# Kernel tuning notes

Measured on AMD Instinct MI355X. Metric: run time of the kernel, lower is better.

The kernel has to match this reference:

```python
import jax, jax.numpy as jnp
import numpy as np

N_NODES = 100000
NEG_SLOPE = 0.2


def glorot(key, shape):
    fan_in, fan_out = shape[0], shape[-1]
    lim = jnp.sqrt(6.0 / (fan_in + fan_out))
    return jax.random.uniform(key, shape, jnp.float32, -lim, lim)


def setup_inputs() -> dict:
    key = jax.random.key(0)
    ks = jax.random.split(key, 16)
    x = jax.random.normal(ks[0], (N_NODES, 128), jnp.float32)
    edge_index = jax.random.randint(ks[1], (2, 1600000), 0, N_NODES, jnp.int64)
    H1, C1 = 4, 32
    C2 = 64
    return {
        "x": x,
        "edge_index": edge_index,
        # layer 1: GATv2Conv(128 -> 32, heads=4, concat)
        "Wl1": glorot(ks[2], (128, H1 * C1)), "bl1": jnp.zeros((H1 * C1,), jnp.float32),
        "Wr1": glorot(ks[3], (128, H1 * C1)), "br1": jnp.zeros((H1 * C1,), jnp.float32),
        "att1": glorot(ks[4], (H1, C1)),
        "bias1": jnp.zeros((H1 * C1,), jnp.float32),
        # layer 2: GATv2Conv(128 -> 64, heads=1, concat)
        "Wl2": glorot(ks[5], (H1 * C1, C2)), "bl2": jnp.zeros((C2,), jnp.float32),
        "Wr2": glorot(ks[6], (H1 * C1, C2)), "br2": jnp.zeros((C2,), jnp.float32),
        "att2": glorot(ks[7], (1, C2)),
        "bias2": jnp.zeros((C2,), jnp.float32),
    }


def gatv2_layer(x, src, dst, Wl, bl, Wr, br, att, bias):
    # x: [N, F_in]; src/dst: [E] (self-loops already appended)
    H, C = att.shape
    n = x.shape[0]
    xl = (x @ Wl + bl).reshape(n, H, C)  # source transform
    xr = (x @ Wr + br).reshape(n, H, C)  # target transform
    e = jax.nn.leaky_relu(xl[src] + xr[dst], NEG_SLOPE)          # [E, H, C]
    score = jnp.einsum('ehc,hc->eh', e, att)                     # [E, H]
    # segment softmax over incoming edges of each destination node
    smax = jax.ops.segment_max(score, dst, num_segments=n)       # [N, H]
    ex = jnp.exp(score - smax[dst])
    denom = jax.ops.segment_sum(ex, dst, num_segments=n)
    alpha = ex / denom[dst]                                      # [E, H]
    out = jax.ops.segment_sum(alpha[:, :, None] * xl[src], dst, num_segments=n)
    return out.reshape(n, H * C) + bias


def reference(x, edge_index, Wl1, bl1, Wr1, br1, att1, bias1,
              Wl2, bl2, Wr2, br2, att2, bias2):
    n = x.shape[0]
    loops = jnp.arange(n, dtype=edge_index.dtype)
    src = jnp.concatenate([edge_index[0], loops])
    dst = jnp.concatenate([edge_index[1], loops])
    h = gatv2_layer(x, src, dst, Wl1, bl1, Wr1, br1, att1, bias1)
    h = jax.nn.relu(h)
    out = gatv2_layer(h, src, dst, Wl2, bl2, Wr2, br2, att2, bias2)
    return out
```

## Files before the change

### kernel.cpp

```cpp
#include <hip/hip_runtime.h>
#include <hip/hip_fp16.h>

#define NEG 0.2f

typedef _Float16 f16x8 __attribute__((ext_vector_type(8)));
typedef _Float16 f16x2 __attribute__((ext_vector_type(2)));
typedef float    f32x4 __attribute__((ext_vector_type(4)));

__device__ __forceinline__ float fdot2h(__half2 a, __half2 b, float c) {
    return __builtin_amdgcn_fdot2(__builtin_bit_cast(f16x2, a),
                                  __builtin_bit_cast(f16x2, b), c, false);
}

__device__ __forceinline__ __half2 u2h2(unsigned int u) {
    return __builtin_bit_cast(__half2, u);
}

__device__ __forceinline__ __half2 hmax2(__half2 a, __half2 b) {
    unsigned int ua = __builtin_bit_cast(unsigned int, a);
    unsigned int ub = __builtin_bit_cast(unsigned int, b);
    unsigned int ud;
    asm("v_pk_max_f16 %0, %1, %2" : "=v"(ud) : "v"(ua), "v"(ub));
    return __builtin_bit_cast(__half2, ud);
}

template<int CTRL>
__device__ __forceinline__ float dppadd(float x) {
    int xi = __builtin_bit_cast(int, x);
    int yi = __builtin_amdgcn_update_dpp(0, xi, CTRL, 0xf, 0xf, true);
    return x + __builtin_bit_cast(float, yi);
}

template<int CGRP, int CPW, bool IN_F16, bool HPL>
__global__ __launch_bounds__(256) void xform_k(
    const float* __restrict__ Xf, const __half* __restrict__ Xh,
    const float* __restrict__ Wl, const float* __restrict__ bl,
    const float* __restrict__ Wr, const float* __restrict__ br,
    __half* __restrict__ YL, __half* __restrict__ YR, int nrows)
{
    __shared__ _Float16 Ws[CGRP * 136];

    const int t  = threadIdx.x;
    const int c0 = blockIdx.y * CGRP;

    for (int i = t; i < 128 * CGRP; i += 256) {
        int k = i / CGRP, cl = i % CGRP;
        int gc = c0 + cl;
        const float* Wp = (gc >= CPW) ? Wr : Wl;
        int lc = gc - ((gc >= CPW) ? CPW : 0);
        Ws[cl * 136 + k] = (_Float16)Wp[(long)k * CPW + lc];
    }
    __syncthreads();

    const int lane = t & 63, wv = t >> 6;
    const int m = lane & 15, quad = lane >> 4;

    const int ntiles = (nrows + 15) >> 4;
    const int stride = gridDim.x * 4;

    int tile = blockIdx.x * 4 + wv;
    if (tile >= ntiles) return;

    f16x8 A0[4], A1[4];

    auto loadA = [&](int tl, f16x8* Af) {
        int row = tl * 16 + m;
        if (row >= nrows) row = nrows - 1;
        if constexpr (IN_F16) {
            const uint4* Xp = (const uint4*)(Xh + (long)row * 128);
            #pragma unroll
            for (int ks = 0; ks < 4; ++ks) {
                uint4 v = Xp[ks * 4 + quad];
                Af[ks] = __builtin_bit_cast(f16x8, v);
            }
        } else {
            const float4* Xp = (const float4*)(Xf + (long)row * 128);
            #pragma unroll
            for (int ks = 0; ks < 4; ++ks) {
                float4 a = Xp[ks * 8 + quad * 2];
                float4 b = Xp[ks * 8 + quad * 2 + 1];
                _Float16 h[8] = {(_Float16)a.x,(_Float16)a.y,(_Float16)a.z,(_Float16)a.w,
                                 (_Float16)b.x,(_Float16)b.y,(_Float16)b.z,(_Float16)b.w};
                Af[ks] = *(f16x8*)h;
            }
        }
    };

    loadA(tile, A0);

    for (; tile < ntiles; tile += stride) {
        int nt = tile + stride;
        if (nt < ntiles) loadA(nt, A1);

        const int r = tile * 16 + m;
        const bool rv = r < nrows;

        #pragma unroll
        for (int ct = 0; ct < CGRP / 16; ++ct) {
            f32x4 acc = (f32x4){0.f, 0.f, 0.f, 0.f};
            #pragma unroll
            for (int ks = 0; ks < 4; ++ks) {
                f16x8 Bf = *(const f16x8*)&Ws[(ct * 16 + m) * 136 + ks * 32 + quad * 8];
                acc = __builtin_amdgcn_mfma_f32_16x16x32_f16(Bf, A0[ks], acc, 0, 0, 0);
            }
            int colb = c0 + ct * 16 + quad * 4;
            int which = colb >= CPW;
            int lcb = colb - (which ? CPW : 0);
            const float* bp = (which ? br : bl) + lcb;
            float4 bb = *(const float4*)bp;
            if (rv) {
                _Float16 h4[4] = { (_Float16)(acc[0] + bb.x), (_Float16)(acc[1] + bb.y),
                                   (_Float16)(acc[2] + bb.z), (_Float16)(acc[3] + bb.w) };
                _Float16* Y = (_Float16*)(which ? YR : YL);
                long idx;
                if (HPL && !which)
                    idx = (long)(lcb >> 6) * ((long)nrows * 64) + (long)r * 64 + (lcb & 63);
                else
                    idx = (long)r * CPW + lcb;
                *(uint2*)&Y[idx] = *(uint2*)h4;
            }
        }
        #pragma unroll
        for (int ks = 0; ks < 4; ++ks) A0[ks] = A1[ks];
    }
}

__global__ __launch_bounds__(256) void h1_k(
    const int* __restrict__ ei, int* __restrict__ gh, int E0, int ET, int NBK)
{
    __shared__ int h[256];
    const int t = threadIdx.x, blk = blockIdx.x;
    h[t] = 0;
    __syncthreads();
    int e = blk * 4096 + t;
    #pragma unroll
    for (int u = 0; u < 16; ++u, e += 256) {
        if (e < ET) {
            int dst = (e < E0) ? ei[E0 + e] : (e - E0);
            atomicAdd(&h[dst >> 9], 1);
        }
    }
    __syncthreads();
    gh[t * NBK + blk] = h[t];
}

__global__ __launch_bounds__(256) void scan1_k(
    const int* __restrict__ cnt, int* __restrict__ loc, int* __restrict__ bsum, int n)
{
    __shared__ int wsum[4];
    int t = threadIdx.x;
    int i0 = blockIdx.x * 1024 + t * 4;
    int4 v;
    v.x = (i0 + 0 < n) ? cnt[i0 + 0] : 0;
    v.y = (i0 + 1 < n) ? cnt[i0 + 1] : 0;
    v.z = (i0 + 2 < n) ? cnt[i0 + 2] : 0;
    v.w = (i0 + 3 < n) ? cnt[i0 + 3] : 0;
    int tsum = v.x + v.y + v.z + v.w;
    int incl = tsum;
    #pragma unroll
    for (int s = 1; s < 64; s <<= 1) {
        int u = __shfl_up(incl, s, 64);
        if ((t & 63) >= s) incl += u;
    }
    int wid = t >> 6;
    if ((t & 63) == 63) wsum[wid] = incl;
    __syncthreads();
    int woff = 0;
    #pragma unroll
    for (int w = 0; w < 4; ++w) if (w < wid) woff += wsum[w];
    int ex = woff + incl - tsum;
    if (i0 + 0 < n) loc[i0 + 0] = ex;
    if (i0 + 1 < n) loc[i0 + 1] = ex + v.x;
    if (i0 + 2 < n) loc[i0 + 2] = ex + v.x + v.y;
    if (i0 + 3 < n) loc[i0 + 3] = ex + v.x + v.y + v.z;
    if (t == 255) bsum[blockIdx.x] = woff + incl;
}

__global__ void scan2_k(const int* __restrict__ bsum, int* __restrict__ bcarry,
                        int M, int* __restrict__ total_out)
{
    int lane = threadIdx.x;
    int carry = 0;
    for (int base = 0; base < M; base += 64) {
        int i = base + lane;
        int v = (i < M) ? bsum[i] : 0;
        int incl = v;
        #pragma unroll
        for (int s = 1; s < 64; s <<= 1) {
            int u = __shfl_up(incl, s, 64);
            if (lane >= s) incl += u;
        }
        if (i < M) bcarry[i] = carry + incl - v;
        carry += __shfl(incl, 63, 64);
    }
    if (lane == 0) *total_out = carry;
}

__global__ __launch_bounds__(256) void scan3_k(
    int* __restrict__ off, const int* __restrict__ bcarry, int n)
{
    int i = blockIdx.x * 256 + threadIdx.x;
    if (i >= n) return;
    off[i] += bcarry[i >> 10];
}

__global__ __launch_bounds__(256) void sc1_k(
    const int* __restrict__ ei, const int* __restrict__ gh,
    uint2* __restrict__ rec, int E0, int ET, int NBK)
{
    __shared__ int lofs[256];
    const int t = threadIdx.x, blk = blockIdx.x;
    lofs[t] = gh[t * NBK + blk];
    __syncthreads();
    int e = blk * 4096 + t;
    #pragma unroll
    for (int u = 0; u < 16; ++u, e += 256) {
        if (e < ET) {
            int src = (e < E0) ? ei[e]      : (e - E0);
            int dst = (e < E0) ? ei[E0 + e] : (e - E0);
            int p = atomicAdd(&lofs[dst >> 9], 1);
            rec[p] = make_uint2((unsigned)src, (unsigned)dst);
        }
    }
}

__global__ __launch_bounds__(256) void p2_k(
    const uint2* __restrict__ rec, const int* __restrict__ gh,
    int* __restrict__ srcs, int* __restrict__ off, int N, int NBK)
{
    __shared__ int hist[512];
    __shared__ int sc[2][512];
    __shared__ int curo[512];
    const int t = threadIdx.x;
    const int b = blockIdx.x;
    const int base = gh[b * NBK];
    const int end  = gh[(b + 1) * NBK];
    hist[t] = 0; hist[t + 256] = 0;
    __syncthreads();
    for (int i = base + t; i < end; i += 256) {
        uint2 r = rec[i];
        atomicAdd(&hist[r.y & 511], 1);
    }
    __syncthreads();
    sc[0][t] = hist[t]; sc[0][t + 256] = hist[t + 256];
    __syncthreads();
    int pp = 0;
    for (int s = 1; s < 512; s <<= 1, pp ^= 1) {
        int j0 = t, j1 = t + 256;
        sc[pp ^ 1][j0] = sc[pp][j0] + ((j0 >= s) ? sc[pp][j0 - s] : 0);
        sc[pp ^ 1][j1] = sc[pp][j1] + ((j1 >= s) ? sc[pp][j1 - s] : 0);
        __syncthreads();
    }
    {
        int j0 = t, j1 = t + 256;
        int e0 = base + sc[pp][j0] - hist[j0];
        int e1 = base + sc[pp][j1] - hist[j1];
        curo[j0] = e0;
        curo[j1] = e1;
        int d0 = b * 512 + j0, d1 = b * 512 + j1;
        if (d0 < N) off[d0] = e0;
        if (d1 < N) off[d1] = e1;
    }
    __syncthreads();
    for (int i = base + t; i < end; i += 256) {
        uint2 r = rec[i];
        int pos = atomicAdd(&curo[r.y & 511], 1);
        srcs[pos] = (int)r.x;
    }
}

template<bool RELU>
__global__ __launch_bounds__(256) void fused128hp_k(
    const __half* __restrict__ XLp, const __half* __restrict__ XR,
    const float* __restrict__ ATT, const int* __restrict__ srcs,
    const int* __restrict__ off, const float* __restrict__ bias,
    __half* __restrict__ OUT, int N, int p)
{
    const int t   = threadIdx.x;
    const int d   = blockIdx.x * 32 + (t >> 3);
    const int sub = t & 7;
    const bool nv = d < N;

    int a = 0, b = 0;
    if (nv) { a = off[d]; b = off[d + 1]; }

    __half2 xr[4] = { u2h2(0), u2h2(0), u2h2(0), u2h2(0) };
    if (nv) {
        uint4 ur = *(const uint4*)(XR + (long)d * 128 + p * 64 + sub * 8);
        xr[0] = u2h2(ur.x); xr[1] = u2h2(ur.y); xr[2] = u2h2(ur.z); xr[3] = u2h2(ur.w);
    }
    float4 at0f = ((const float4*)ATT)[p * 16 + sub * 2];
    float4 at1f = ((const float4*)ATT)[p * 16 + sub * 2 + 1];
    __half2 at[4] = { __floats2half2_rn(at0f.x, at0f.y), __floats2half2_rn(at0f.z, at0f.w),
                      __floats2half2_rn(at1f.x, at1f.y), __floats2half2_rn(at1f.z, at1f.w) };
    const __half2 neg2 = __float2half2_rn(NEG);

    float l = 0.f;
    float accv[8] = {0.f,0.f,0.f,0.f,0.f,0.f,0.f,0.f};

    const uint4* XL4 = (const uint4*)(XLp + (size_t)p * N * 64);

    if (b > a) {
        const int bm1 = b - 1;
        int sA = srcs[a];
        uint4 r0 = XL4[(long)sA * 8 + sub];
        int i1 = (a + 1 < bm1) ? a + 1 : bm1;
        int sB = srcs[i1];
        uint4 r1 = XL4[(long)sB * 8 + sub];
        int i2 = (a + 2 < bm1) ? a + 2 : bm1;
        int s2 = srcs[i2];

        for (int e = a; e < b; ++e) {
            uint4 r2 = XL4[(long)s2 * 8 + sub];
            int i3 = (e + 3 < bm1) ? e + 3 : bm1;
            int s3 = srcs[i3];

            __half2 x0 = u2h2(r0.x), x1 = u2h2(r0.y), x2 = u2h2(r0.z), x3 = u2h2(r0.w);
            __half2 s0h = __hadd2(x0, xr[0]);
            __half2 s1h = __hadd2(x1, xr[1]);
            __half2 s2h = __hadd2(x2, xr[2]);
            __half2 s3h = __hadd2(x3, xr[3]);
            __half2 q0 = hmax2(s0h, __hmul2(s0h, neg2));
            __half2 q1 = hmax2(s1h, __hmul2(s1h, neg2));
            __half2 q2 = hmax2(s2h, __hmul2(s2h, neg2));
            __half2 q3 = hmax2(s3h, __hmul2(s3h, neg2));
            float p0 = fdot2h(q0, at[0], 0.f);
            p0 = fdot2h(q1, at[1], p0);
            p0 = fdot2h(q2, at[2], p0);
            p0 = fdot2h(q3, at[3], p0);
            p0 = dppadd<0xB1>(p0);
            p0 = dppadd<0x4E>(p0);
            float ex = __expf(p0);
            l += ex;
            float2 f0 = __half22float2(x0), f1 = __half22float2(x1);
            float2 f2 = __half22float2(x2), f3 = __half22float2(x3);
            accv[0] += ex * f0.x; accv[1] += ex * f0.y;
            accv[2] += ex * f1.x; accv[3] += ex * f1.y;
            accv[4] += ex * f2.x; accv[5] += ex * f2.y;
            accv[6] += ex * f3.x; accv[7] += ex * f3.y;

            r0 = r1; r1 = r2; s2 = s3;
        }
    }

    if (nv) {
        float inv = 1.f / l;
        float4 b0 = ((const float4*)bias)[p * 16 + sub * 2];
        float4 b1 = ((const float4*)bias)[p * 16 + sub * 2 + 1];
        float o[8] = { accv[0]*inv + b0.x, accv[1]*inv + b0.y,
                       accv[2]*inv + b0.z, accv[3]*inv + b0.w,
                       accv[4]*inv + b1.x, accv[5]*inv + b1.y,
                       accv[6]*inv + b1.z, accv[7]*inv + b1.w };
        if constexpr (RELU) {
            #pragma unroll
            for (int j = 0; j < 8; ++j) o[j] = fmaxf(o[j], 0.f);
        }
        uint4 uo;
        uo.x = __builtin_bit_cast(unsigned int, __floats2half2_rn(o[0], o[1]));
        uo.y = __builtin_bit_cast(unsigned int, __floats2half2_rn(o[2], o[3]));
        uo.z = __builtin_bit_cast(unsigned int, __floats2half2_rn(o[4], o[5]));
        uo.w = __builtin_bit_cast(unsigned int, __floats2half2_rn(o[6], o[7]));
        *(uint4*)(OUT + (long)d * 128 + p * 64 + sub * 8) = uo;
    }
}

template<bool RELU>
__global__ __launch_bounds__(256) void fused64_k(
    const __half* __restrict__ XL, const __half* __restrict__ XR,
    const float* __restrict__ ATT, const int* __restrict__ srcs,
    const int* __restrict__ off, const float* __restrict__ bias,
    float* __restrict__ OUT, int N)
{
    const int t   = threadIdx.x;
    const int d   = blockIdx.x * 32 + (t >> 3);
    const int sub = t & 7;
    const bool nv = d < N;

    int a = 0, b = 0;
    if (nv) { a = off[d]; b = off[d + 1]; }

    __half2 xr[4] = { u2h2(0), u2h2(0), u2h2(0), u2h2(0) };
    if (nv) {
        uint4 ur = *(const uint4*)(XR + (long)d * 64 + sub * 8);
        xr[0] = u2h2(ur.x); xr[1] = u2h2(ur.y); xr[2] = u2h2(ur.z); xr[3] = u2h2(ur.w);
    }
    float4 at0f = ((const float4*)ATT)[sub * 2];
    float4 at1f = ((const float4*)ATT)[sub * 2 + 1];
    __half2 at[4] = { __floats2half2_rn(at0f.x, at0f.y), __floats2half2_rn(at0f.z, at0f.w),
                      __floats2half2_rn(at1f.x, at1f.y), __floats2half2_rn(at1f.z, at1f.w) };
    const __half2 neg2 = __float2half2_rn(NEG);

    float l = 0.f;
    float accv[8] = {0.f,0.f,0.f,0.f,0.f,0.f,0.f,0.f};

    const uint4* XL4 = (const uint4*)XL;

    if (b > a) {
        const int bm1 = b - 1;
        int sA = srcs[a];
        uint4 r0 = XL4[(long)sA * 8 + sub];
        int i1 = (a + 1 < bm1) ? a + 1 : bm1;
        int sB = srcs[i1];
        uint4 r1 = XL4[(long)sB * 8 + sub];
        int i2 = (a + 2 < bm1) ? a + 2 : bm1;
        int s2 = srcs[i2];

        for (int e = a; e < b; ++e) {
            uint4 r2 = XL4[(long)s2 * 8 + sub];
            int i3 = (e + 3 < bm1) ? e + 3 : bm1;
            int s3 = srcs[i3];

            __half2 x0 = u2h2(r0.x), x1 = u2h2(r0.y), x2 = u2h2(r0.z), x3 = u2h2(r0.w);
            __half2 s0h = __hadd2(x0, xr[0]);
            __half2 s1h = __hadd2(x1, xr[1]);
            __half2 s2h = __hadd2(x2, xr[2]);
            __half2 s3h = __hadd2(x3, xr[3]);
            __half2 q0 = hmax2(s0h, __hmul2(s0h, neg2));
            __half2 q1 = hmax2(s1h, __hmul2(s1h, neg2));
            __half2 q2 = hmax2(s2h, __hmul2(s2h, neg2));
            __half2 q3 = hmax2(s3h, __hmul2(s3h, neg2));
            float p0 = fdot2h(q0, at[0], 0.f);
            p0 = fdot2h(q1, at[1], p0);
            p0 = fdot2h(q2, at[2], p0);
            p0 = fdot2h(q3, at[3], p0);
            p0 = dppadd<0xB1>(p0);
            p0 = dppadd<0x4E>(p0);
            p0 = dppadd<0x141>(p0);
            float ex = __expf(p0);
            l += ex;
            float2 f0 = __half22float2(x0), f1 = __half22float2(x1);
            float2 f2 = __half22float2(x2), f3 = __half22float2(x3);
            accv[0] += ex * f0.x; accv[1] += ex * f0.y;
            accv[2] += ex * f1.x; accv[3] += ex * f1.y;
            accv[4] += ex * f2.x; accv[5] += ex * f2.y;
            accv[6] += ex * f3.x; accv[7] += ex * f3.y;

            r0 = r1; r1 = r2; s2 = s3;
        }
    }

    if (nv) {
        float inv = 1.f / l;
        float4 b0 = ((const float4*)bias)[sub * 2];
        float4 b1 = ((const float4*)bias)[sub * 2 + 1];
        float4 o0 = make_float4(accv[0]*inv + b0.x, accv[1]*inv + b0.y,
                                accv[2]*inv + b0.z, accv[3]*inv + b0.w);
        float4 o1 = make_float4(accv[4]*inv + b1.x, accv[5]*inv + b1.y,
                                accv[6]*inv + b1.z, accv[7]*inv + b1.w);
        if constexpr (RELU) {
            o0.x = fmaxf(o0.x, 0.f); o0.y = fmaxf(o0.y, 0.f);
            o0.z = fmaxf(o0.z, 0.f); o0.w = fmaxf(o0.w, 0.f);
            o1.x = fmaxf(o1.x, 0.f); o1.y = fmaxf(o1.y, 0.f);
            o1.z = fmaxf(o1.z, 0.f); o1.w = fmaxf(o1.w, 0.f);
        }
        *(float4*)(OUT + (long)d * 64 + sub * 8)     = o0;
        *(float4*)(OUT + (long)d * 64 + sub * 8 + 4) = o1;
    }
}

extern "C" void kernel_launch(void* const* d_in, const int* in_sizes, int n_in,
                              void* d_out, int out_size, void* d_ws, size_t ws_size,
                              hipStream_t stream)
{
    const float* x     = (const float*)d_in[0];
    const int*   ei    = (const int*)  d_in[1];
    const float* Wl1   = (const float*)d_in[2];
    const float* bl1   = (const float*)d_in[3];
    const float* Wr1   = (const float*)d_in[4];
    const float* br1   = (const float*)d_in[5];
    const float* att1  = (const float*)d_in[6];
    const float* bias1 = (const float*)d_in[7];
    const float* Wl2   = (const float*)d_in[8];
    const float* bl2   = (const float*)d_in[9];
    const float* Wr2   = (const float*)d_in[10];
    const float* br2   = (const float*)d_in[11];
    const float* att2  = (const float*)d_in[12];
    const float* bias2 = (const float*)d_in[13];

    const int  N  = in_sizes[0] / 128;
    const int  E0 = in_sizes[1] / 2;
    const int  ET = E0 + N;

    char* w = (char*)d_ws;
    __half* XLh = (__half*)w;
    __half* XRh = XLh + (size_t)N * 128;
    __half* Cch = XRh + (size_t)N * 128;
    int*    off = (int*)(Cch + (size_t)N * 128);
    int*    srcs= off + (N + 1);
    int*    gh  = srcs + ET;
    uint2*  rec = (uint2*)w;
    float*  out = (float*)d_out;

    dim3 b256(256);
    const int ng32  = (N + 31) / 32;

    const int NBK   = (ET + 4095) / 4096;
    const int n1    = 256 * NBK;
    const int NB1   = (n1 + 1023) / 1024;
    const int NBUCK = (N + 511) / 512;
    int* bsum = gh + n1;
    int* bcar = bsum + NB1;

    h1_k<<<NBK, b256, 0, stream>>>(ei, gh, E0, ET, NBK);
    scan1_k<<<NB1, b256, 0, stream>>>(gh, gh, bsum, n1);
    scan2_k<<<1, 64, 0, stream>>>(bsum, bcar, NB1, off + N);
    scan3_k<<<(n1 + 255) / 256, b256, 0, stream>>>(gh, bcar, n1);
    sc1_k<<<NBK, b256, 0, stream>>>(ei, gh, rec, E0, ET, NBK);
    p2_k<<<NBUCK, b256, 0, stream>>>(rec, gh, srcs, off, N, NBK);

    xform_k<128, 128, false, true><<<dim3(512, 2), b256, 0, stream>>>(
        x, nullptr, Wl1, bl1, Wr1, br1, XLh, XRh, N);
    fused128hp_k<true><<<ng32, b256, 0, stream>>>(XLh, XRh, att1, srcs, off, bias1, Cch, N, 0);
    fused128hp_k<true><<<ng32, b256, 0, stream>>>(XLh, XRh, att1, srcs, off, bias1, Cch, N, 1);

    xform_k<128, 64, true, false><<<dim3(1024, 1), b256, 0, stream>>>(
        nullptr, Cch, Wl2, bl2, Wr2, br2, XLh, XRh, N);
    fused64_k<false><<<ng32, b256, 0, stream>>>(XLh, XRh, att2, srcs, off, bias2, out, N);
}
```

Measured before the change: 380.1 us.

## Compute all output columns per block in xform and deepen A prefetch

The layer-1 transform now computes all 256 output columns (Wl and Wr) in one block instead of splitting the columns across two grid rows. Each X tile is therefore read once instead of twice. The weight staging uses float4 loads and a 140-element LDS row pitch, and the A-fragment prefetch goes from one tile ahead to two. The cost is more LDS per block (about 70KB for layer 1) and more registers, which can lower occupancy. The layer-2 grid is also halved to 512 blocks.

```diff
diff --git a/kernel.cpp b/kernel.cpp
--- a/kernel.cpp
+++ b/kernel.cpp
@@ -31,24 +31,27 @@
     return x + __builtin_bit_cast(float, yi);
 }
 
-template<int CGRP, int CPW, bool IN_F16, bool HPL>
+template<int COLS, int CPW, bool IN_F16, bool HPL>
 __global__ __launch_bounds__(256) void xform_k(
     const float* __restrict__ Xf, const __half* __restrict__ Xh,
     const float* __restrict__ Wl, const float* __restrict__ bl,
     const float* __restrict__ Wr, const float* __restrict__ br,
     __half* __restrict__ YL, __half* __restrict__ YR, int nrows)
 {
-    __shared__ _Float16 Ws[CGRP * 136];
-
-    const int t  = threadIdx.x;
-    const int c0 = blockIdx.y * CGRP;
-
-    for (int i = t; i < 128 * CGRP; i += 256) {
-        int k = i / CGRP, cl = i % CGRP;
-        int gc = c0 + cl;
-        const float* Wp = (gc >= CPW) ? Wr : Wl;
-        int lc = gc - ((gc >= CPW) ? CPW : 0);
-        Ws[cl * 136 + k] = (_Float16)Wp[(long)k * CPW + lc];
+    __shared__ _Float16 Ws[COLS * 140];
+
+    const int t = threadIdx.x;
+
+    for (int i = t; i < 128 * (COLS / 4); i += 256) {
+        int k  = i / (COLS / 4);
+        int c4 = (i % (COLS / 4)) * 4;
+        const float* Wp = (c4 >= CPW) ? Wr : Wl;
+        int lc = c4 - ((c4 >= CPW) ? CPW : 0);
+        float4 v = *(const float4*)&Wp[(long)k * CPW + lc];
+        Ws[(c4 + 0) * 140 + k] = (_Float16)v.x;
+        Ws[(c4 + 1) * 140 + k] = (_Float16)v.y;
+        Ws[(c4 + 2) * 140 + k] = (_Float16)v.z;
+        Ws[(c4 + 3) * 140 + k] = (_Float16)v.w;
     }
     __syncthreads();
 
@@ -61,7 +64,7 @@
     int tile = blockIdx.x * 4 + wv;
     if (tile >= ntiles) return;
 
-    f16x8 A0[4], A1[4];
+    f16x8 A0[4], A1[4], A2[4];
 
     auto loadA = [&](int tl, f16x8* Af) {
         int row = tl * 16 + m;
@@ -87,23 +90,24 @@
     };
 
     loadA(tile, A0);
+    if (tile + stride < ntiles) loadA(tile + stride, A1);
 
     for (; tile < ntiles; tile += stride) {
-        int nt = tile + stride;
-        if (nt < ntiles) loadA(nt, A1);
+        int nt2 = tile + 2 * stride;
+        if (nt2 < ntiles) loadA(nt2, A2);
 
         const int r = tile * 16 + m;
         const bool rv = r < nrows;
 
         #pragma unroll
-        for (int ct = 0; ct < CGRP / 16; ++ct) {
+        for (int ct = 0; ct < COLS / 16; ++ct) {
             f32x4 acc = (f32x4){0.f, 0.f, 0.f, 0.f};
             #pragma unroll
             for (int ks = 0; ks < 4; ++ks) {
-                f16x8 Bf = *(const f16x8*)&Ws[(ct * 16 + m) * 136 + ks * 32 + quad * 8];
+                f16x8 Bf = *(const f16x8*)&Ws[(ct * 16 + m) * 140 + ks * 32 + quad * 8];
                 acc = __builtin_amdgcn_mfma_f32_16x16x32_f16(Bf, A0[ks], acc, 0, 0, 0);
             }
-            int colb = c0 + ct * 16 + quad * 4;
+            int colb = ct * 16 + quad * 4;
             int which = colb >= CPW;
             int lcb = colb - (which ? CPW : 0);
             const float* bp = (which ? br : bl) + lcb;
@@ -121,7 +125,7 @@
             }
         }
         #pragma unroll
-        for (int ks = 0; ks < 4; ++ks) A0[ks] = A1[ks];
+        for (int ks = 0; ks < 4; ++ks) { A0[ks] = A1[ks]; A1[ks] = A2[ks]; }
     }
 }
 
@@ -508,12 +512,12 @@
     sc1_k<<<NBK, b256, 0, stream>>>(ei, gh, rec, E0, ET, NBK);
     p2_k<<<NBUCK, b256, 0, stream>>>(rec, gh, srcs, off, N, NBK);
 
-    xform_k<128, 128, false, true><<<dim3(512, 2), b256, 0, stream>>>(
+    xform_k<256, 128, false, true><<<512, b256, 0, stream>>>(
         x, nullptr, Wl1, bl1, Wr1, br1, XLh, XRh, N);
     fused128hp_k<true><<<ng32, b256, 0, stream>>>(XLh, XRh, att1, srcs, off, bias1, Cch, N, 0);
     fused128hp_k<true><<<ng32, b256, 0, stream>>>(XLh, XRh, att1, srcs, off, bias1, Cch, N, 1);
 
-    xform_k<128, 64, true, false><<<dim3(1024, 1), b256, 0, stream>>>(
+    xform_k<128, 64, true, false><<<512, b256, 0, stream>>>(
         nullptr, Cch, Wl2, bl2, Wr2, br2, XLh, XRh, N);
     fused64_k<false><<<ng32, b256, 0, stream>>>(XLh, XRh, att2, srcs, off, bias2, out, N);
 }
```

Result: slower. 392.6 us (+3.3%).
